# Performance work log

Measured on AMD Instinct MI355X. Metric: run time of the kernel, lower is better.

Reference implementation:

```python
import jax, jax.numpy as jnp
import numpy as np

B, N, F_IN = 32, 1024, 128
H1, H2, OUT = 64, 32, 10
EDGE_P = 0.01  # edge probability for random adjacency


def setup_inputs() -> dict:
    key = jax.random.key(0)
    ks = jax.random.split(key, 16)
    x = jax.random.normal(ks[0], (B, N, F_IN), dtype=jnp.float32)
    # dense binary adjacency per graph (module consumes dense [N,N] adj)
    adj = (jax.random.uniform(ks[1], (B, N, N)) < EDGE_P).astype(jnp.float32)
    mask = jnp.ones((B, N, 1), dtype=jnp.float32)
    s = 0.05
    W1a = jax.random.normal(ks[2], (F_IN, H1), dtype=jnp.float32) * s
    b1a = jnp.zeros((H1,), dtype=jnp.float32)
    W2a = jax.random.normal(ks[3], (H1, H1), dtype=jnp.float32) * s
    b2a = jnp.zeros((H1,), dtype=jnp.float32)
    W1b = jax.random.normal(ks[4], (H1, H2), dtype=jnp.float32) * s
    b1b = jnp.zeros((H2,), dtype=jnp.float32)
    W2b = jax.random.normal(ks[5], (H2, H2), dtype=jnp.float32) * s
    b2b = jnp.zeros((H2,), dtype=jnp.float32)
    Wfc = jax.random.normal(ks[6], (H2, OUT), dtype=jnp.float32) * s
    bfc = jnp.zeros((OUT,), dtype=jnp.float32)
    return dict(x=x, adj=adj, mask=mask, W1a=W1a, b1a=b1a, W2a=W2a, b2a=b2a,
                W1b=W1b, b1b=b1b, W2b=W2b, b2b=b2b, Wfc=Wfc, bfc=bfc)


def _gin_layer(h, adj, mask, Wa, ba, Wb, bb, eps=0.0):
    # neighbor sum aggregation: neigh[b,i] = sum_j adj[b,i,j] * h[b,j]
    neigh = jnp.einsum('bij,bjf->bif', adj, h)
    z = (1.0 + eps) * h + neigh
    z = jax.nn.relu(z @ Wa + ba) @ Wb + bb  # 2-layer MLP
    return z * mask  # zero out padded nodes


def reference(x, adj, mask, W1a, b1a, W2a, b2a, W1b, b1b, W2b, b2b, Wfc, bfc):
    h = _gin_layer(x, adj, mask, W1a, b1a, W2a, b2a)   # [B,N,64]
    h = _gin_layer(h, adj, mask, W1b, b1b, W2b, b2b)   # [B,N,32]
    g = jnp.max(h, axis=1)                              # graph readout [B,32]
    return g @ Wfc + bfc                                # [B,OUT] (dropout = eval identity)
```

## Files before the change

kernel.cpp:

```cpp
#include <hip/hip_runtime.h>
#include <cstdint>
#include <cstddef>


#define CAP 64

typedef float v4f __attribute__((ext_vector_type(4)));

__device__ __forceinline__ float rl(float x, int l) {
  return __int_as_float(__builtin_amdgcn_readlane(__float_as_int(x), l));
}

__global__ __launch_bounds__(256) void k_scanproj(
    const float* __restrict__ x, const float* __restrict__ W1a,
    float* __restrict__ u,
    const float* __restrict__ adj, unsigned short* __restrict__ nbr,
    int* __restrict__ deg, unsigned* __restrict__ g_u32) {
  int lane = threadIdx.x & 63;
  int wid  = threadIdx.x >> 6;
  if (blockIdx.x == 0) {
    #pragma unroll
    for (int i = 0; i < 4; ++i) g_u32[threadIdx.x * 4 + i] = 0u;
  }
  if (blockIdx.x < 1024) {
    int row0 = (blockIdx.x * 4 + wid) * 8;
    row0 = __builtin_amdgcn_readfirstlane(row0);
    const float* xr = x + (size_t)row0 * 128;
    float acc[8] = {0, 0, 0, 0, 0, 0, 0, 0};
    for (int kc = 0; kc < 32; ++kc) {
      v4f xv[8];
      #pragma unroll
      for (int r = 0; r < 8; ++r)
        xv[r] = *(const v4f*)(xr + r * 128 + kc * 4);
      #pragma unroll
      for (int j = 0; j < 4; ++j) {
        float w = W1a[(kc * 4 + j) * 64 + lane];
        #pragma unroll
        for (int r = 0; r < 8; ++r)
          acc[r] = fmaf(xv[r][j], w, acc[r]);
      }
    }
    #pragma unroll
    for (int r = 0; r < 8; ++r)
      u[(size_t)(row0 + r) * 64 + lane] = acc[r];
  } else {
    int node = (blockIdx.x - 1024) * 8 + wid * 2;
    const v4f* arow0 = (const v4f*)(adj + (size_t)node * 1024);
    const v4f* arow1 = (const v4f*)(adj + ((size_t)node + 1) * 1024);
    unsigned short* outp0 = nbr + node * CAP;
    unsigned short* outp1 = outp0 + CAP;
    v4f a0[4], a1[4];
    #pragma unroll
    for (int c = 0; c < 4; ++c) {
      a0[c] = __builtin_nontemporal_load(arow0 + c * 64 + lane);
      a1[c] = __builtin_nontemporal_load(arow1 + c * 64 + lane);
    }
    int cnt0 = 0, cnt1 = 0;
    #pragma unroll
    for (int c = 0; c < 4; ++c) {
      #pragma unroll
      for (int comp = 0; comp < 4; ++comp) {
        int idx = ((c * 64 + lane) << 2) + comp;
        bool h0 = (a0[c][comp] != 0.0f);
        bool h1 = (a1[c][comp] != 0.0f);
        unsigned long long m0 = __ballot(h0);
        unsigned long long m1 = __ballot(h1);
        if (h0) {
          int below = __builtin_amdgcn_mbcnt_hi(
              (unsigned)(m0 >> 32),
              __builtin_amdgcn_mbcnt_lo((unsigned)m0, 0));
          int pos = cnt0 + below;
          if (pos < CAP) outp0[pos] = (unsigned short)idx;
        }
        if (h1) {
          int below = __builtin_amdgcn_mbcnt_hi(
              (unsigned)(m1 >> 32),
              __builtin_amdgcn_mbcnt_lo((unsigned)m1, 0));
          int pos = cnt1 + below;
          if (pos < CAP) outp1[pos] = (unsigned short)idx;
        }
        cnt0 += __popcll(m0);
        cnt1 += __popcll(m1);
      }
    }
    if (lane == 0) {
      deg[node]     = cnt0 < CAP ? cnt0 : CAP;
      deg[node + 1] = cnt1 < CAP ? cnt1 : CAP;
    }
  }
}

__global__ __launch_bounds__(256) void k_gathA(
    const float* __restrict__ u, const unsigned short* __restrict__ nbr,
    const int* __restrict__ deg, const float* __restrict__ mask,
    const float* __restrict__ b1a, const float* __restrict__ W2a,
    const float* __restrict__ b2a, const float* __restrict__ W1b,
    float* __restrict__ v) {
  __shared__ float sW2[64 * 64];
  __shared__ float sW1b[64 * 32];
  float wr2[16], wr1[8];
  #pragma unroll
  for (int i = 0; i < 16; ++i) wr2[i] = W2a[threadIdx.x + i * 256];
  #pragma unroll
  for (int i = 0; i < 8; ++i)  wr1[i] = W1b[threadIdx.x + i * 256];
  int lane = threadIdx.x & 63;
  int f = lane & 31, hh = lane >> 5;
  float ba1 = b1a[lane], ba2 = b2a[lane];
  int i = blockIdx.x, wid = threadIdx.x >> 6;
  int xcd = i & 7, j = i >> 3;
  int b = xcd + 8 * (j & 3);
  int w = j >> 2;
  int n0 = b * 1024 + w * 8 + wid * 2, n1 = n0 + 1;
  const float* ub = u + (size_t)b * 1024 * 64;
  int d0 = deg[n0], d1 = deg[n1];
  int nl0 = nbr[n0 * CAP + lane], nl1 = nbr[n1 * CAP + lane];
  float self0 = ub[(n0 & 1023) * 64 + lane];
  float self1 = ub[(n1 & 1023) * 64 + lane];
  float s0[8] = {0,0,0,0,0,0,0,0}, s1[8] = {0,0,0,0,0,0,0,0};
  int dmax = d0 > d1 ? d0 : d1;
  int rounds = (dmax + 7) >> 3;
  for (int rr = 0; rr < rounds; ++rr) {
    int base = rr << 3;
    #pragma unroll
    for (int i2 = 0; i2 < 8; ++i2) {
      int t = base + i2;
      int j0 = __builtin_amdgcn_readlane(nl0, t);
      int j1 = __builtin_amdgcn_readlane(nl1, t);
      bool ok0 = t < d0, ok1 = t < d1;
      j0 = ok0 ? j0 : 0;  j1 = ok1 ? j1 : 0;
      float v0 = ub[j0 * 64 + lane];
      float v1 = ub[j1 * 64 + lane];
      s0[i2] += ok0 ? v0 : 0.0f;
      s1[i2] += ok1 ? v1 : 0.0f;
    }
  }
  float acc0 = self0
             + (((s0[0]+s0[1])+(s0[2]+s0[3]))+((s0[4]+s0[5])+(s0[6]+s0[7])));
  float acc1 = self1
             + (((s1[0]+s1[1])+(s1[2]+s1[3]))+((s1[4]+s1[5])+(s1[6]+s1[7])));
  #pragma unroll
  for (int t = 0; t < 16; ++t) sW2[threadIdx.x + t * 256] = wr2[t];
  #pragma unroll
  for (int t = 0; t < 8; ++t)  sW1b[threadIdx.x + t * 256] = wr1[t];
  __syncthreads();
  float r0 = fmaxf(acc0 + ba1, 0.0f);
  float r1 = fmaxf(acc1 + ba1, 0.0f);
  float a0=0,a1=0,a2=0,a3=0, c0=0,c1=0,c2=0,c3=0;
  #pragma unroll
  for (int k = 0; k < 64; k += 4) {
    float w0 = sW2[(k    ) * 64 + lane];
    float w1 = sW2[(k + 1) * 64 + lane];
    float w2 = sW2[(k + 2) * 64 + lane];
    float w3 = sW2[(k + 3) * 64 + lane];
    a0 = fmaf(rl(r0, k    ), w0, a0);  c0 = fmaf(rl(r1, k    ), w0, c0);
    a1 = fmaf(rl(r0, k + 1), w1, a1);  c1 = fmaf(rl(r1, k + 1), w1, c1);
    a2 = fmaf(rl(r0, k + 2), w2, a2);  c2 = fmaf(rl(r1, k + 2), w2, c2);
    a3 = fmaf(rl(r0, k + 3), w3, a3);  c3 = fmaf(rl(r1, k + 3), w3, c3);
  }
  float h20 = (ba2 + ((a0 + a1) + (a2 + a3))) * mask[n0];
  float h21 = (ba2 + ((c0 + c1) + (c2 + c3))) * mask[n1];
  float p00=0,p01=0, p10=0,p11=0;
  #pragma unroll
  for (int k0 = 0; k0 < 32; k0 += 2) {
    float w0 = sW1b[(hh * 32 + k0    ) * 32 + f];
    float w1 = sW1b[(hh * 32 + k0 + 1) * 32 + f];
    p00 = fmaf(__shfl(h20, hh * 32 + k0    ), w0, p00);
    p01 = fmaf(__shfl(h20, hh * 32 + k0 + 1), w1, p01);
    p10 = fmaf(__shfl(h21, hh * 32 + k0    ), w0, p10);
    p11 = fmaf(__shfl(h21, hh * 32 + k0 + 1), w1, p11);
  }
  float vp0 = p00 + p01;  vp0 += __shfl_xor(vp0, 32);
  float vp1 = p10 + p11;  vp1 += __shfl_xor(vp1, 32);
  if (hh == 0) {
    v[n0 * 32 + f] = vp0;
    v[n1 * 32 + f] = vp1;
  }
}

__global__ __launch_bounds__(256) void k_gathB(
    const float* __restrict__ v, const unsigned short* __restrict__ nbr,
    const int* __restrict__ deg, const float* __restrict__ mask,
    const float* __restrict__ b1b, const float* __restrict__ W2b,
    const float* __restrict__ b2b, unsigned* __restrict__ g_u32) {
  __shared__ float sW2b[32 * 32];
  __shared__ float wred[4][32];
  float wrb[4];
  #pragma unroll
  for (int i = 0; i < 4; ++i) wrb[i] = W2b[threadIdx.x + i * 256];
  int lane = threadIdx.x & 63;
  int f = lane & 31, hh = lane >> 5;
  float bb1 = b1b[f], bb2 = b2b[f];
  int i = blockIdx.x, wid = threadIdx.x >> 6;
  int xcd = i & 7, j = i >> 3;
  int b = xcd + 8 * (j & 3);
  int w = j >> 2;
  int n0 = b * 1024 + w * 8 + wid * 2, n1 = n0 + 1;
  const float* vb = v + (size_t)b * 1024 * 32;
  int d0 = deg[n0], d1 = deg[n1];
  int nl0 = nbr[n0 * CAP + lane], nl1 = nbr[n1 * CAP + lane];
  float selfv0 = vb[(n0 & 1023) * 32 + f];
  float selfv1 = vb[(n1 & 1023) * 32 + f];
  float s0[8] = {0,0,0,0,0,0,0,0}, s1[8] = {0,0,0,0,0,0,0,0};
  int dmax = d0 > d1 ? d0 : d1;
  int rounds = (dmax + 15) >> 4;
  for (int rr = 0; rr < rounds; ++rr) {
    int base = rr << 4;
    #pragma unroll
    for (int i2 = 0; i2 < 8; ++i2) {
      int t = base + (i2 << 1) + hh;
      int j0 = __shfl(nl0, t);
      int j1 = __shfl(nl1, t);
      bool ok0 = t < d0, ok1 = t < d1;
      j0 = ok0 ? j0 : 0;  j1 = ok1 ? j1 : 0;
      float v0 = vb[j0 * 32 + f];
      float v1 = vb[j1 * 32 + f];
      s0[i2] += ok0 ? v0 : 0.0f;
      s1[i2] += ok1 ? v1 : 0.0f;
    }
  }
  float acc0 = ((s0[0]+s0[1])+(s0[2]+s0[3]))+((s0[4]+s0[5])+(s0[6]+s0[7]));
  float acc1 = ((s1[0]+s1[1])+(s1[2]+s1[3]))+((s1[4]+s1[5])+(s1[6]+s1[7]));
  acc0 += __shfl_xor(acc0, 32);
  acc1 += __shfl_xor(acc1, 32);
  #pragma unroll
  for (int t = 0; t < 4; ++t) sW2b[threadIdx.x + t * 256] = wrb[t];
  __syncthreads();
  float r0 = fmaxf(selfv0 + acc0 + bb1, 0.0f);
  float r1 = fmaxf(selfv1 + acc1 + bb1, 0.0f);
  float a0=0,a1=0,a2=0,a3=0, c0=0,c1=0,c2=0,c3=0;
  #pragma unroll
  for (int k = 0; k < 32; k += 4) {
    float w0 = sW2b[(k    ) * 32 + f];
    float w1 = sW2b[(k + 1) * 32 + f];
    float w2 = sW2b[(k + 2) * 32 + f];
    float w3 = sW2b[(k + 3) * 32 + f];
    a0 = fmaf(rl(r0, k    ), w0, a0);  c0 = fmaf(rl(r1, k    ), w0, c0);
    a1 = fmaf(rl(r0, k + 1), w1, a1);  c1 = fmaf(rl(r1, k + 1), w1, c1);
    a2 = fmaf(rl(r0, k + 2), w2, a2);  c2 = fmaf(rl(r1, k + 2), w2, c2);
    a3 = fmaf(rl(r0, k + 3), w3, a3);  c3 = fmaf(rl(r1, k + 3), w3, c3);
  }
  float o0 = (bb2 + ((a0 + a1) + (a2 + a3))) * mask[n0];
  float o1 = (bb2 + ((c0 + c1) + (c2 + c3))) * mask[n1];
  float m = fmaxf(o0, o1);
  if (hh == 0) wred[wid][f] = m;
  __syncthreads();
  if (threadIdx.x < 32) {
    float mm = fmaxf(fmaxf(wred[0][threadIdx.x], wred[1][threadIdx.x]),
                     fmaxf(wred[2][threadIdx.x], wred[3][threadIdx.x]));
    unsigned bu  = __float_as_uint(mm);
    unsigned key = bu ^ ((unsigned)((int)bu >> 31) | 0x80000000u);
    atomicMax(&g_u32[(b << 5) + threadIdx.x], key);
  }
}

__global__ __launch_bounds__(320) void k_fin(
    const unsigned* __restrict__ g_u32, const float* __restrict__ Wfc,
    const float* __restrict__ bfc, float* __restrict__ out) {
  __shared__ float g[1024];
  int t = threadIdx.x;
  if (t < 256) {
    #pragma unroll
    for (int i = 0; i < 4; ++i) {
      unsigned key  = g_u32[t * 4 + i];
      unsigned flip = (key >> 31) ? 0x80000000u : 0xFFFFFFFFu;
      g[t * 4 + i] = __uint_as_float(key ^ flip);
    }
  }
  __syncthreads();
  int b = t / 10, o = t - b * 10;
  if (b < 32) {
    float acc = bfc[o];
    #pragma unroll
    for (int k = 0; k < 32; ++k)
      acc = fmaf(g[b * 32 + k], Wfc[k * 10 + o], acc);
    out[b * 10 + o] = acc;
  }
}

extern "C" void kernel_launch(void* const* d_in, const int* in_sizes, int n_in,
                              void* d_out, int out_size, void* d_ws, size_t ws_size,
                              hipStream_t stream) {
  const float* x    = (const float*)d_in[0];
  const float* adj  = (const float*)d_in[1];
  const float* mask = (const float*)d_in[2];
  const float* W1a  = (const float*)d_in[3];
  const float* b1a  = (const float*)d_in[4];
  const float* W2a  = (const float*)d_in[5];
  const float* b2a  = (const float*)d_in[6];
  const float* W1b  = (const float*)d_in[7];
  const float* b1b  = (const float*)d_in[8];
  const float* W2b  = (const float*)d_in[9];
  const float* b2b  = (const float*)d_in[10];
  const float* Wfc  = (const float*)d_in[11];
  const float* bfc  = (const float*)d_in[12];
  float* out = (float*)d_out;

  char* ws = (char*)d_ws;
  float*          u     = (float*)(ws);
  float*          v     = (float*)(ws + (8u  << 20));
  unsigned short* nbr   = (unsigned short*)(ws + (12u << 20));
  int*            deg   = (int*)  (ws + (16u << 20));
  unsigned*       g_u32 = (unsigned*)(ws + (17u << 20));

  hipLaunchKernelGGL(k_scanproj, dim3(5120), dim3(256), 0, stream,
                     x, W1a, u, adj, nbr, deg, g_u32);
  hipLaunchKernelGGL(k_gathA,    dim3(4096), dim3(256), 0, stream,
                     u, nbr, deg, mask, b1a, W2a, b2a, W1b, v);
  hipLaunchKernelGGL(k_gathB,    dim3(4096), dim3(256), 0, stream,
                     v, nbr, deg, mask, b1b, W2b, b2b, g_u32);
  hipLaunchKernelGGL(k_fin,      dim3(1),    dim3(320), 0, stream,
                     g_u32, Wfc, bfc, out);
}
```

Measured before the change: 269.3 us.

## Fuse adjacency scan into layer-A gather kernel, split projection out

```diff
diff --git a/kernel.cpp b/kernel.cpp
--- a/kernel.cpp
+++ b/kernel.cpp
@@ -11,93 +11,47 @@
   return __int_as_float(__builtin_amdgcn_readlane(__float_as_int(x), l));
 }
 
-__global__ __launch_bounds__(256) void k_scanproj(
+__global__ __launch_bounds__(256) void k_proj(
     const float* __restrict__ x, const float* __restrict__ W1a,
-    float* __restrict__ u,
-    const float* __restrict__ adj, unsigned short* __restrict__ nbr,
-    int* __restrict__ deg, unsigned* __restrict__ g_u32) {
+    float* __restrict__ u, unsigned* __restrict__ g_u32) {
   int lane = threadIdx.x & 63;
   int wid  = threadIdx.x >> 6;
   if (blockIdx.x == 0) {
     #pragma unroll
     for (int i = 0; i < 4; ++i) g_u32[threadIdx.x * 4 + i] = 0u;
   }
-  if (blockIdx.x < 1024) {
-    int row0 = (blockIdx.x * 4 + wid) * 8;
-    row0 = __builtin_amdgcn_readfirstlane(row0);
-    const float* xr = x + (size_t)row0 * 128;
-    float acc[8] = {0, 0, 0, 0, 0, 0, 0, 0};
-    for (int kc = 0; kc < 32; ++kc) {
-      v4f xv[8];
+  int row0 = (blockIdx.x * 4 + wid) * 8;
+  row0 = __builtin_amdgcn_readfirstlane(row0);
+  const float* xr = x + (size_t)row0 * 128;
+  float acc[8] = {0, 0, 0, 0, 0, 0, 0, 0};
+  for (int kc = 0; kc < 32; ++kc) {
+    v4f xv[8];
+    #pragma unroll
+    for (int r = 0; r < 8; ++r)
+      xv[r] = *(const v4f*)(xr + r * 128 + kc * 4);
+    #pragma unroll
+    for (int j = 0; j < 4; ++j) {
+      float w = W1a[(kc * 4 + j) * 64 + lane];
       #pragma unroll
       for (int r = 0; r < 8; ++r)
-        xv[r] = *(const v4f*)(xr + r * 128 + kc * 4);
-      #pragma unroll
-      for (int j = 0; j < 4; ++j) {
-        float w = W1a[(kc * 4 + j) * 64 + lane];
-        #pragma unroll
-        for (int r = 0; r < 8; ++r)
-          acc[r] = fmaf(xv[r][j], w, acc[r]);
-      }
-    }
-    #pragma unroll
-    for (int r = 0; r < 8; ++r)
-      u[(size_t)(row0 + r) * 64 + lane] = acc[r];
-  } else {
-    int node = (blockIdx.x - 1024) * 8 + wid * 2;
-    const v4f* arow0 = (const v4f*)(adj + (size_t)node * 1024);
-    const v4f* arow1 = (const v4f*)(adj + ((size_t)node + 1) * 1024);
-    unsigned short* outp0 = nbr + node * CAP;
-    unsigned short* outp1 = outp0 + CAP;
-    v4f a0[4], a1[4];
-    #pragma unroll
-    for (int c = 0; c < 4; ++c) {
-      a0[c] = __builtin_nontemporal_load(arow0 + c * 64 + lane);
-      a1[c] = __builtin_nontemporal_load(arow1 + c * 64 + lane);
-    }
-    int cnt0 = 0, cnt1 = 0;
-    #pragma unroll
-    for (int c = 0; c < 4; ++c) {
-      #pragma unroll
-      for (int comp = 0; comp < 4; ++comp) {
-        int idx = ((c * 64 + lane) << 2) + comp;
-        bool h0 = (a0[c][comp] != 0.0f);
-        bool h1 = (a1[c][comp] != 0.0f);
-        unsigned long long m0 = __ballot(h0);
-        unsigned long long m1 = __ballot(h1);
-        if (h0) {
-          int below = __builtin_amdgcn_mbcnt_hi(
-              (unsigned)(m0 >> 32),
-              __builtin_amdgcn_mbcnt_lo((unsigned)m0, 0));
-          int pos = cnt0 + below;
-          if (pos < CAP) outp0[pos] = (unsigned short)idx;
-        }
-        if (h1) {
-          int below = __builtin_amdgcn_mbcnt_hi(
-              (unsigned)(m1 >> 32),
-              __builtin_amdgcn_mbcnt_lo((unsigned)m1, 0));
-          int pos = cnt1 + below;
-          if (pos < CAP) outp1[pos] = (unsigned short)idx;
-        }
-        cnt0 += __popcll(m0);
-        cnt1 += __popcll(m1);
-      }
-    }
-    if (lane == 0) {
-      deg[node]     = cnt0 < CAP ? cnt0 : CAP;
-      deg[node + 1] = cnt1 < CAP ? cnt1 : CAP;
-    }
-  }
-}
-
-__global__ __launch_bounds__(256) void k_gathA(
-    const float* __restrict__ u, const unsigned short* __restrict__ nbr,
-    const int* __restrict__ deg, const float* __restrict__ mask,
+        acc[r] = fmaf(xv[r][j], w, acc[r]);
+    }
+  }
+  #pragma unroll
+  for (int r = 0; r < 8; ++r)
+    u[(size_t)(row0 + r) * 64 + lane] = acc[r];
+}
+
+__global__ __launch_bounds__(256) void k_gathAS(
+    const float* __restrict__ u, const float* __restrict__ adj,
+    const float* __restrict__ mask,
     const float* __restrict__ b1a, const float* __restrict__ W2a,
     const float* __restrict__ b2a, const float* __restrict__ W1b,
-    float* __restrict__ v) {
+    float* __restrict__ v, unsigned short* __restrict__ nbr,
+    int* __restrict__ deg) {
   __shared__ float sW2[64 * 64];
   __shared__ float sW1b[64 * 32];
+  __shared__ unsigned short sIdx[4][2][64];
   float wr2[16], wr1[8];
   #pragma unroll
   for (int i = 0; i < 16; ++i) wr2[i] = W2a[threadIdx.x + i * 256];
@@ -112,10 +66,57 @@
   int w = j >> 2;
   int n0 = b * 1024 + w * 8 + wid * 2, n1 = n0 + 1;
   const float* ub = u + (size_t)b * 1024 * 64;
-  int d0 = deg[n0], d1 = deg[n1];
-  int nl0 = nbr[n0 * CAP + lane], nl1 = nbr[n1 * CAP + lane];
   float self0 = ub[(n0 & 1023) * 64 + lane];
   float self1 = ub[(n1 & 1023) * 64 + lane];
+  const v4f* arow0 = (const v4f*)(adj + (size_t)n0 * 1024);
+  const v4f* arow1 = (const v4f*)(adj + (size_t)n1 * 1024);
+  unsigned short* outp0 = nbr + n0 * CAP;
+  unsigned short* outp1 = outp0 + CAP;
+  v4f a0[4], a1[4];
+  #pragma unroll
+  for (int c = 0; c < 4; ++c) {
+    a0[c] = __builtin_nontemporal_load(arow0 + c * 64 + lane);
+    a1[c] = __builtin_nontemporal_load(arow1 + c * 64 + lane);
+  }
+  int cnt0 = 0, cnt1 = 0;
+  #pragma unroll
+  for (int c = 0; c < 4; ++c) {
+    #pragma unroll
+    for (int comp = 0; comp < 4; ++comp) {
+      int idx = ((c * 64 + lane) << 2) + comp;
+      bool h0 = (a0[c][comp] != 0.0f);
+      bool h1 = (a1[c][comp] != 0.0f);
+      unsigned long long m0 = __ballot(h0);
+      unsigned long long m1 = __ballot(h1);
+      if (h0) {
+        int below = __builtin_amdgcn_mbcnt_hi(
+            (unsigned)(m0 >> 32),
+            __builtin_amdgcn_mbcnt_lo((unsigned)m0, 0));
+        int pos = cnt0 + below;
+        if (pos < CAP) {
+          sIdx[wid][0][pos] = (unsigned short)idx;
+          outp0[pos] = (unsigned short)idx;
+        }
+      }
+      if (h1) {
+        int below = __builtin_amdgcn_mbcnt_hi(
+            (unsigned)(m1 >> 32),
+            __builtin_amdgcn_mbcnt_lo((unsigned)m1, 0));
+        int pos = cnt1 + below;
+        if (pos < CAP) {
+          sIdx[wid][1][pos] = (unsigned short)idx;
+          outp1[pos] = (unsigned short)idx;
+        }
+      }
+      cnt0 += __popcll(m0);
+      cnt1 += __popcll(m1);
+    }
+  }
+  int d0 = cnt0 < CAP ? cnt0 : CAP;
+  int d1 = cnt1 < CAP ? cnt1 : CAP;
+  if (lane == 0) { deg[n0] = d0; deg[n1] = d1; }
+  int nl0 = sIdx[wid][0][lane];
+  int nl1 = sIdx[wid][1][lane];
   float s0[8] = {0,0,0,0,0,0,0,0}, s1[8] = {0,0,0,0,0,0,0,0};
   int dmax = d0 > d1 ? d0 : d1;
   int rounds = (dmax + 7) >> 3;
@@ -145,20 +146,20 @@
   __syncthreads();
   float r0 = fmaxf(acc0 + ba1, 0.0f);
   float r1 = fmaxf(acc1 + ba1, 0.0f);
-  float a0=0,a1=0,a2=0,a3=0, c0=0,c1=0,c2=0,c3=0;
+  float a0f=0,a1f=0,a2f=0,a3f=0, c0f=0,c1f=0,c2f=0,c3f=0;
   #pragma unroll
   for (int k = 0; k < 64; k += 4) {
     float w0 = sW2[(k    ) * 64 + lane];
     float w1 = sW2[(k + 1) * 64 + lane];
     float w2 = sW2[(k + 2) * 64 + lane];
     float w3 = sW2[(k + 3) * 64 + lane];
-    a0 = fmaf(rl(r0, k    ), w0, a0);  c0 = fmaf(rl(r1, k    ), w0, c0);
-    a1 = fmaf(rl(r0, k + 1), w1, a1);  c1 = fmaf(rl(r1, k + 1), w1, c1);
-    a2 = fmaf(rl(r0, k + 2), w2, a2);  c2 = fmaf(rl(r1, k + 2), w2, c2);
-    a3 = fmaf(rl(r0, k + 3), w3, a3);  c3 = fmaf(rl(r1, k + 3), w3, c3);
-  }
-  float h20 = (ba2 + ((a0 + a1) + (a2 + a3))) * mask[n0];
-  float h21 = (ba2 + ((c0 + c1) + (c2 + c3))) * mask[n1];
+    a0f = fmaf(rl(r0, k    ), w0, a0f);  c0f = fmaf(rl(r1, k    ), w0, c0f);
+    a1f = fmaf(rl(r0, k + 1), w1, a1f);  c1f = fmaf(rl(r1, k + 1), w1, c1f);
+    a2f = fmaf(rl(r0, k + 2), w2, a2f);  c2f = fmaf(rl(r1, k + 2), w2, c2f);
+    a3f = fmaf(rl(r0, k + 3), w3, a3f);  c3f = fmaf(rl(r1, k + 3), w3, c3f);
+  }
+  float h20 = (ba2 + ((a0f + a1f) + (a2f + a3f))) * mask[n0];
+  float h21 = (ba2 + ((c0f + c1f) + (c2f + c3f))) * mask[n1];
   float p00=0,p01=0, p10=0,p11=0;
   #pragma unroll
   for (int k0 = 0; k0 < 32; k0 += 2) {
@@ -302,12 +303,12 @@
   int*            deg   = (int*)  (ws + (16u << 20));
   unsigned*       g_u32 = (unsigned*)(ws + (17u << 20));
 
-  hipLaunchKernelGGL(k_scanproj, dim3(5120), dim3(256), 0, stream,
-                     x, W1a, u, adj, nbr, deg, g_u32);
-  hipLaunchKernelGGL(k_gathA,    dim3(4096), dim3(256), 0, stream,
-                     u, nbr, deg, mask, b1a, W2a, b2a, W1b, v);
-  hipLaunchKernelGGL(k_gathB,    dim3(4096), dim3(256), 0, stream,
+  hipLaunchKernelGGL(k_proj,   dim3(1024), dim3(256), 0, stream,
+                     x, W1a, u, g_u32);
+  hipLaunchKernelGGL(k_gathAS, dim3(4096), dim3(256), 0, stream,
+                     u, adj, mask, b1a, W2a, b2a, W1b, v, nbr, deg);
+  hipLaunchKernelGGL(k_gathB,  dim3(4096), dim3(256), 0, stream,
                      v, nbr, deg, mask, b1b, W2b, b2b, g_u32);
-  hipLaunchKernelGGL(k_fin,      dim3(1),    dim3(320), 0, stream,
+  hipLaunchKernelGGL(k_fin,    dim3(1),    dim3(320), 0, stream,
                      g_u32, Wfc, bfc, out);
 }
```

Result: no change. 274.3 us (+1.9%).
